# Performance work log

Measured on AMD Instinct MI355X. Metric: run time of the kernel, lower is better.

The kernel has to match this reference:

```python
import jax, jax.numpy as jnp
import numpy as np

B, T_STEPS, H, W = 8192, 512, 64, 64


def setup_inputs() -> dict:
    key = jax.random.key(0)
    k_w, k_g, k_i, k_j, k_a = jax.random.split(key, 5)
    walls = (jax.random.uniform(k_w, (B, H, W)) < 0.3).astype(jnp.float32)
    walls = walls.at[:, 0, :].set(1.0).at[:, H - 1, :].set(1.0)
    walls = walls.at[:, :, 0].set(1.0).at[:, :, W - 1].set(1.0)
    # goals: sparse cells with value 10 (the code checks goals[...] == 10)
    goals = jnp.where(jax.random.uniform(k_g, (B, H, W)) < 0.02, 10.0, 0.0).astype(jnp.float32)
    # start positions strictly interior; clear the wall at each start cell
    i0 = jax.random.randint(k_i, (B,), 1, H - 1)
    j0 = jax.random.randint(k_j, (B,), 1, W - 1)
    walls = walls.at[jnp.arange(B), i0, j0].set(0.0)
    world = jnp.stack([walls, goals], axis=1)  # [B, 2, H, W]
    s0 = jnp.stack([i0, j0], axis=1).astype(jnp.float32)  # [B, 2]
    a = jax.random.randint(k_a, (B, T_STEPS), 0, 5).astype(jnp.int32)  # actions in {0..4}
    return {"s0": s0, "a": a, "world": world, "T": T_STEPS}


def _rollout(s0, a, world, T):
    walls = world[:, 0].reshape(world.shape[0], -1)  # [B, H*W]
    goals = world[:, 1].reshape(world.shape[0], -1)  # [B, H*W]
    Wd = world.shape[3]

    def step(s, a_t):
        # action deltas: 1 -> row-1, 2 -> row+1, 3 -> col-1, 4 -> col+1, 0 -> stay
        dr = jnp.where(a_t == 1, -1.0, jnp.where(a_t == 2, 1.0, 0.0))
        dc = jnp.where(a_t == 3, -1.0, jnp.where(a_t == 4, 1.0, 0.0))
        s_new = s + jnp.stack([dr, dc], axis=1).astype(s.dtype)  # [B, 2]
        idx = (s_new[:, 0].astype(jnp.int32) * Wd + s_new[:, 1].astype(jnp.int32))[:, None]
        g = jnp.take_along_axis(goals, idx, axis=1)[:, 0]
        w = jnp.take_along_axis(walls, idx, axis=1)[:, 0]
        hit_goal = g == 10.0
        hit_wall = jnp.logical_and(jnp.logical_not(hit_goal), w == 1.0)
        r = jnp.where(hit_goal, 1.0, jnp.where(hit_wall, -1.0, -0.01)).astype(jnp.float32)
        s_next = jnp.where(hit_wall[:, None], s, s_new)  # revert move on wall hit
        return s_next, (s_next, r)

    _, (s_traj, r_traj) = jax.lax.scan(step, s0, jnp.swapaxes(a[:, :T], 0, 1))
    s_full = jnp.concatenate([s0[:, None, :], jnp.swapaxes(s_traj, 0, 1)], axis=1)  # [B, T+1, 2]
    r0 = jnp.zeros((s0.shape[0], 1), dtype=jnp.float32)
    r_full = jnp.concatenate([r0, jnp.swapaxes(r_traj, 0, 1)], axis=1)  # [B, T+1]
    return s_full, r_full


def reference(s0, a, world, T):
    return _rollout(s0, a, world, T)
```

## Files before the change

### kernel.cpp

```cpp
#include <hip/hip_runtime.h>
#include <stdint.h>

#define T_STEPS 512
#define CELLS   4096
#define EPB     32
#define WPE     256
#define WPAD    257
#define AWORDS  128
#define ASTRIDE 130

__device__ __forceinline__ uint32_t code4(float4 w, float4 g) {
    uint32_t b0 = (g.x == 10.0f) ? 2u : ((w.x == 1.0f) ? 1u : 0u);
    uint32_t b1 = (g.y == 10.0f) ? 2u : ((w.y == 1.0f) ? 1u : 0u);
    uint32_t b2 = (g.z == 10.0f) ? 2u : ((w.z == 1.0f) ? 1u : 0u);
    uint32_t b3 = (g.w == 10.0f) ? 2u : ((w.w == 1.0f) ? 1u : 0u);
    return b0 | (b1 << 2) | (b2 << 4) | (b3 << 6);
}

__global__ __launch_bounds__(64) void pack_kernel(
    const float* __restrict__ world, uint32_t* __restrict__ packed)
{
    const int b = blockIdx.x;
    const int t = threadIdx.x;
    const float* wbase = world + (size_t)b * (2 * CELLS);
    const float* gbase = wbase + CELLS;
    #pragma unroll
    for (int h = 0; h < 4; ++h) {
        const int w  = h * 64 + t;
        const int c0 = w * 16;
        uint32_t word = 0;
        #pragma unroll
        for (int j = 0; j < 4; ++j) {
            float4 wf = *(const float4*)(wbase + c0 + 4 * j);
            float4 gf = *(const float4*)(gbase + c0 + 4 * j);
            word |= code4(wf, gf) << (8 * j);
        }
        packed[(size_t)b * WPE + w] = word;
    }
}

__global__ __launch_bounds__(64) void rollout_kernel(
    const float* __restrict__ s0,
    const int*   __restrict__ act,
    const uint32_t* __restrict__ packed,
    float* __restrict__ out,
    int B)
{
    __shared__ uint32_t wlds[EPB * WPAD];
    __shared__ uint32_t alds[EPB * ASTRIDE];

    const int tid = threadIdx.x;
    const int b0  = blockIdx.x * EPB;

    for (int ee = 0; ee < EPB; ++ee) {
        uint4 v = *(const uint4*)(packed + (size_t)(b0 + ee) * WPE + tid * 4);
        const int base = ee * WPAD + tid * 4;
        wlds[base]     = v.x;
        wlds[base + 1] = v.y;
        wlds[base + 2] = v.z;
        wlds[base + 3] = v.w;
    }
    for (int ee = 0; ee < EPB; ++ee) {
        const int4* ap = (const int4*)(act + (size_t)(b0 + ee) * T_STEPS);
        const int4 x = ap[2 * tid];
        const int4 y = ap[2 * tid + 1];
        const uint32_t w0 = (uint32_t)(x.x & 255) | ((uint32_t)(x.y & 255) << 8)
                          | ((uint32_t)(x.z & 255) << 16) | ((uint32_t)(x.w & 255) << 24);
        const uint32_t w1 = (uint32_t)(y.x & 255) | ((uint32_t)(y.y & 255) << 8)
                          | ((uint32_t)(y.z & 255) << 16) | ((uint32_t)(y.w & 255) << 24);
        const int base = ee * ASTRIDE + 2 * tid;
        alds[base]     = w0;
        alds[base + 1] = w1;
    }
    __syncthreads();

    if (tid < EPB) {
        const int b = b0 + tid;
        float2 s = *(const float2*)(s0 + 2 * (size_t)b);
        int r = (int)s.x;
        int c = (int)s.y;
        int p = r * 64 + c;
        const uint32_t* my    = wlds + tid * WPAD;
        const uint32_t* myact = alds + tid * ASTRIDE;

        auto lookup = [&](int q) -> int {
            const int idx = q + ((q < 0) ? CELLS : 0);
            const uint32_t wd = my[(idx >> 4) & (WPE - 1)];
            const int cell = (wd >> ((idx & 15) * 2)) & 3;
            return ((unsigned)idx < (unsigned)CELLS) ? cell : 0;
        };

        float* s_out = out + (size_t)b * (2 * (T_STEPS + 1));
        float* r_out = out + (size_t)B * (2 * (T_STEPS + 1)) + (size_t)b * (T_STEPS + 1);

        *(float2*)s_out = s;
        r_out[0] = 0.0f;

        uint32_t aw = myact[0];
        for (int k = 0; k < T_STEPS / 4; ++k) {
            const uint32_t aw_next = myact[k + 1];
            const int a0 = aw & 255, a1 = (aw >> 8) & 255;
            const int a2 = (aw >> 16) & 255, a3 = (aw >> 24) & 255;
            const int as4[4] = {a0, a1, a2, a3};
            #pragma unroll
            for (int jj = 0; jj < 2; ++jj) {
                const int t  = k * 4 + jj * 2;
                const int u0 = as4[2 * jj];
                const int u1 = as4[2 * jj + 1];
                const int d0r = (u0 == 1) ? -1 : ((u0 == 2) ? 1 : 0);
                const int d0c = (u0 == 3) ? -1 : ((u0 == 4) ? 1 : 0);
                const int d1r = (u1 == 1) ? -1 : ((u1 == 2) ? 1 : 0);
                const int d1c = (u1 == 3) ? -1 : ((u1 == 4) ? 1 : 0);
                const int e0 = d0r * 64 + d0c;
                const int e1 = d1r * 64 + d1c;
                const int q0  = p + e0;
                const int q10 = p + e1;
                const int q11 = q0 + e1;
                const int l0  = lookup(q0);
                const int l10 = lookup(q10);
                const int l11 = lookup(q11);
                const bool hw0  = (l0 == 1);
                const float rew0 = (l0 == 2) ? 1.0f : (hw0 ? -1.0f : -0.01f);
                const int p0  = hw0 ? p : q0;
                const int r0v = hw0 ? r : r + d0r;
                const int c0v = hw0 ? c : c + d0c;
                const int l1 = hw0 ? l10 : l11;
                const bool hw1  = (l1 == 1);
                const float rew1 = (l1 == 2) ? 1.0f : (hw1 ? -1.0f : -0.01f);
                p = hw1 ? p0 : p0 + e1;
                r = hw1 ? r0v : r0v + d1r;
                c = hw1 ? c0v : c0v + d1c;
                *(float2*)(s_out + 2 * (t + 1)) = make_float2((float)r0v, (float)c0v);
                *(float2*)(s_out + 2 * (t + 2)) = make_float2((float)r, (float)c);
                r_out[t + 1] = rew0;
                r_out[t + 2] = rew1;
            }
            aw = aw_next;
        }
    }
}

extern "C" void kernel_launch(void* const* d_in, const int* in_sizes, int n_in,
                              void* d_out, int out_size, void* d_ws, size_t ws_size,
                              hipStream_t stream) {
    const float* s0    = (const float*)d_in[0];
    const int*   act   = (const int*)d_in[1];
    const float* world = (const float*)d_in[2];
    float*       out   = (float*)d_out;
    uint32_t*    packed = (uint32_t*)d_ws;

    const int B = in_sizes[0] / 2;

    pack_kernel<<<B, 64, 0, stream>>>(world, packed);
    rollout_kernel<<<B / EPB, 64, 0, stream>>>(s0, act, packed, out, B);
}
```

Measured before the change: 450.3 us.

## Stage rollout outputs in LDS per chunk and write them coalesced

Per-step state and reward outputs go into shared-memory buffers in 32-step chunks instead of straight to global memory. After each chunk, all 64 threads copy the buffers to global memory in contiguous runs, replacing the scattered per-lane float2 and float stores whose addresses were far apart. To make that possible, the upper 32 lanes now run the same serial rollout as the lower 32, which duplicates work. It also adds two block barriers per chunk to the serial step chain.

```diff
diff --git a/kernel.cpp b/kernel.cpp
--- a/kernel.cpp
+++ b/kernel.cpp
@@ -6,8 +6,12 @@
 #define EPB     32
 #define WPE     256
 #define WPAD    257
-#define AWORDS  128
 #define ASTRIDE 130
+#define SSTRIDE 66
+#define RSTRIDE 33
+#define CHUNK   32
+#define NCHUNK  (T_STEPS / CHUNK)
+#define KPC     (CHUNK / 4)
 
 __device__ __forceinline__ uint32_t code4(float4 w, float4 g) {
     uint32_t b0 = (g.x == 10.0f) ? 2u : ((w.x == 1.0f) ? 1u : 0u);
@@ -48,6 +52,8 @@
 {
     __shared__ uint32_t wlds[EPB * WPAD];
     __shared__ uint32_t alds[EPB * ASTRIDE];
+    __shared__ float    sbuf[EPB * SSTRIDE];
+    __shared__ float    rbuf[EPB * RSTRIDE];
 
     const int tid = threadIdx.x;
     const int b0  = blockIdx.x * EPB;
@@ -74,37 +80,41 @@
     }
     __syncthreads();
 
+    const int e = tid & (EPB - 1);
+    const int b = b0 + e;
+    float2 s = *(const float2*)(s0 + 2 * (size_t)b);
+    int r = (int)s.x;
+    int c = (int)s.y;
+    int p = r * 64 + c;
+    const uint32_t* my    = wlds + e * WPAD;
+    const uint32_t* myact = alds + e * ASTRIDE;
+
+    auto lookup = [&](int q) -> int {
+        const int idx = q + ((q < 0) ? CELLS : 0);
+        const uint32_t wd = my[(idx >> 4) & (WPE - 1)];
+        const int cell = (wd >> ((idx & 15) * 2)) & 3;
+        return ((unsigned)idx < (unsigned)CELLS) ? cell : 0;
+    };
+
+    float* const s_base = out;
+    float* const r_base = out + (size_t)B * (2 * (T_STEPS + 1));
+
     if (tid < EPB) {
-        const int b = b0 + tid;
-        float2 s = *(const float2*)(s0 + 2 * (size_t)b);
-        int r = (int)s.x;
-        int c = (int)s.y;
-        int p = r * 64 + c;
-        const uint32_t* my    = wlds + tid * WPAD;
-        const uint32_t* myact = alds + tid * ASTRIDE;
+        *(float2*)(s_base + (size_t)b * (2 * (T_STEPS + 1))) = s;
+        r_base[(size_t)b * (T_STEPS + 1)] = 0.0f;
+    }
 
-        auto lookup = [&](int q) -> int {
-            const int idx = q + ((q < 0) ? CELLS : 0);
-            const uint32_t wd = my[(idx >> 4) & (WPE - 1)];
-            const int cell = (wd >> ((idx & 15) * 2)) & 3;
-            return ((unsigned)idx < (unsigned)CELLS) ? cell : 0;
-        };
-
-        float* s_out = out + (size_t)b * (2 * (T_STEPS + 1));
-        float* r_out = out + (size_t)B * (2 * (T_STEPS + 1)) + (size_t)b * (T_STEPS + 1);
-
-        *(float2*)s_out = s;
-        r_out[0] = 0.0f;
-
-        uint32_t aw = myact[0];
-        for (int k = 0; k < T_STEPS / 4; ++k) {
-            const uint32_t aw_next = myact[k + 1];
+    uint32_t aw = myact[0];
+    for (int chunk = 0; chunk < NCHUNK; ++chunk) {
+        for (int k = 0; k < KPC; ++k) {
+            const int kk = chunk * KPC + k;
+            const uint32_t aw_next = myact[kk + 1];
             const int a0 = aw & 255, a1 = (aw >> 8) & 255;
             const int a2 = (aw >> 16) & 255, a3 = (aw >> 24) & 255;
             const int as4[4] = {a0, a1, a2, a3};
             #pragma unroll
             for (int jj = 0; jj < 2; ++jj) {
-                const int t  = k * 4 + jj * 2;
+                const int ls = k * 4 + jj * 2;
                 const int u0 = as4[2 * jj];
                 const int u1 = as4[2 * jj + 1];
                 const int d0r = (u0 == 1) ? -1 : ((u0 == 2) ? 1 : 0);
@@ -130,13 +140,27 @@
                 p = hw1 ? p0 : p0 + e1;
                 r = hw1 ? r0v : r0v + d1r;
                 c = hw1 ? c0v : c0v + d1c;
-                *(float2*)(s_out + 2 * (t + 1)) = make_float2((float)r0v, (float)c0v);
-                *(float2*)(s_out + 2 * (t + 2)) = make_float2((float)r, (float)c);
-                r_out[t + 1] = rew0;
-                r_out[t + 2] = rew1;
+                *(float2*)(&sbuf[e * SSTRIDE + 2 * ls]) =
+                    make_float2((float)r0v, (float)c0v);
+                *(float2*)(&sbuf[e * SSTRIDE + 2 * ls + 2]) =
+                    make_float2((float)r, (float)c);
+                rbuf[e * RSTRIDE + ls]     = rew0;
+                rbuf[e * RSTRIDE + ls + 1] = rew1;
             }
             aw = aw_next;
         }
+        __syncthreads();
+        for (int ee = 0; ee < EPB; ++ee) {
+            const float v = sbuf[ee * SSTRIDE + tid];
+            s_base[(size_t)(b0 + ee) * (2 * (T_STEPS + 1)) + chunk * 64 + 2 + tid] = v;
+        }
+        for (int ee = 0; ee < EPB; ee += 2) {
+            const int e2 = ee + (tid >> 5);
+            const int j  = tid & 31;
+            const float v = rbuf[e2 * RSTRIDE + j];
+            r_base[(size_t)(b0 + e2) * (T_STEPS + 1) + chunk * 32 + 1 + j] = v;
+        }
+        __syncthreads();
     }
 }
 
```

Result: no change. 443.8 us (-1.4%).
